# Kernel optimization log

Measured on AMD Instinct MI355X. Metric: run time of the kernel, lower is better.

The kernel has to match this reference:

```python
import jax, jax.numpy as jnp
import numpy as np

N_BLADES = 32  # Cl(4,1) has 2^5 = 32 basis blades


def _gp_sign_bitwise(a, b):
    """Sign of e_a * e_b in Cl(4,1) via bitwise swap counting (numpy, static)."""
    a = np.asarray(a, dtype=np.int64)
    b = np.asarray(b, dtype=np.int64)
    a, b = np.broadcast_arrays(a, b)
    swaps = np.zeros(a.shape, dtype=np.int64)
    for i in range(5):
        b_has_i = (b >> i) & 1
        mask_gt = (~((1 << (i + 1)) - 1)) & 31
        val = a & mask_gt
        pc = (val & 1) + ((val >> 1) & 1) + ((val >> 2) & 1) + ((val >> 3) & 1) + ((val >> 4) & 1)
        swaps += b_has_i * pc
    comm_sign = np.where(swaps % 2 == 0, 1.0, -1.0)
    metric_sign = np.where(((a & 16) & (b & 16)) > 0, -1.0, 1.0)
    return (comm_sign * metric_sign).astype(np.float32)


_M = np.arange(N_BLADES)
PERM = (_M[:, None] ^ _M[None, :]).astype(np.int32)        # PERM[k, m] = m ^ k
SIGNS = _gp_sign_bitwise(_M[None, :], PERM)                 # sign(m, m^k), [32, 32]
PERM_J = jnp.asarray(PERM)
SIGNS_J = jnp.asarray(SIGNS)


def setup_inputs() -> dict:
    key = jax.random.key(0)
    kx, kw = jax.random.split(key)
    B, In, Out = 1024, 256, 256
    x = jax.random.normal(kx, (B, In, N_BLADES), dtype=jnp.float32)
    std = 0.5 / (In * N_BLADES) ** 0.5
    weight = jax.random.normal(kw, (Out, In, N_BLADES), dtype=jnp.float32) * std
    return {"x": x, "weight": weight}


def reference(x, weight):
    # x: [B, In, 32], weight: [Out, In, 32]
    # out[b, o, k] = sum_{i, m} x[b, i, m^k] * sign(m, m^k) * w[o, i, m]
    x_g = x[..., PERM_J] * SIGNS_J                 # [B, In, 32(k), 32(m)]
    out = jnp.einsum('bikm,oim->bok', x_g, weight)  # [B, Out, 32]
    return out
```

## Files before the change

### kernel.cpp

```cpp
#include <hip/hip_runtime.h>

typedef __attribute__((ext_vector_type(8))) short bf16x8;
typedef __attribute__((ext_vector_type(16))) float f32x16;
typedef __attribute__((ext_vector_type(8))) unsigned short ushort8;

#define N_BLADES 32
#define B_DIM 1024
#define IN_DIM 256
#define OUT_DIM 256
#define K_DIM (IN_DIM * N_BLADES)
#define N_DIM (OUT_DIM * N_BLADES)


__device__ __forceinline__ unsigned short f2bf(float f) {
    unsigned int u = __float_as_uint(f);
    u = (u + 0x7fff + ((u >> 16) & 1)) >> 16;
    return (unsigned short)u;
}

__device__ __forceinline__ float gp_sign(int a, int b) {
    int swaps = 0;
#pragma unroll
    for (int i = 0; i < 5; ++i) {
        int mask = (~((1 << (i + 1)) - 1)) & 31;
        swaps += ((b >> i) & 1) * __popc(a & mask);
    }
    float s = (swaps & 1) ? -1.0f : 1.0f;
    if (a & b & 16) s = -s;
    return s;
}

__device__ __forceinline__ void gload_lds16(const void* g, void* l) {
    __builtin_amdgcn_global_load_lds(
        (const __attribute__((address_space(1))) unsigned int*)g,
        (__attribute__((address_space(3))) unsigned int*)l, 16, 0, 0);
}

#define FENCE() asm volatile("" ::: "memory")
#define BAR()    { FENCE(); __builtin_amdgcn_s_barrier(); FENCE(); }
#define SCHED0() __builtin_amdgcn_sched_barrier(0)
#define LGKM(n)  { asm volatile("s_waitcnt lgkmcnt(" #n ")" ::: "memory"); }
#define VMC(n)   { asm volatile("s_waitcnt vmcnt(" #n ")" ::: "memory"); }

__global__ __launch_bounds__(256) void cast_kernel(const float4* __restrict__ x,
                                                   unsigned short* __restrict__ xb) {
    int t = blockIdx.x * 256 + threadIdx.x;
    float4 a = x[t * 2];
    float4 b = x[t * 2 + 1];
    ushort8 pk;
    pk[0] = f2bf(a.x); pk[1] = f2bf(a.y); pk[2] = f2bf(a.z); pk[3] = f2bf(a.w);
    pk[4] = f2bf(b.x); pk[5] = f2bf(b.y); pk[6] = f2bf(b.z); pk[7] = f2bf(b.w);
    *(ushort8*)(xb + (size_t)t * 8) = pk;
}

__device__ __forceinline__ bf16x8 shuffle_sign(bf16x8 v, int jx,
                                               unsigned int m0, unsigned int m1,
                                               unsigned int m2, unsigned int m3) {
    union { bf16x8 v8; unsigned int w[4]; } a, b;
    a.v8 = v;
    int s = jx >> 1;
    unsigned int t0 = (s & 1) ? a.w[1] : a.w[0];
    unsigned int t1 = (s & 1) ? a.w[0] : a.w[1];
    unsigned int t2 = (s & 1) ? a.w[3] : a.w[2];
    unsigned int t3 = (s & 1) ? a.w[2] : a.w[3];
    unsigned int u0 = (s & 2) ? t2 : t0;
    unsigned int u1 = (s & 2) ? t3 : t1;
    unsigned int u2 = (s & 2) ? t0 : t2;
    unsigned int u3 = (s & 2) ? t1 : t3;
    if (jx & 1) {
        u0 = (u0 >> 16) | (u0 << 16);
        u1 = (u1 >> 16) | (u1 << 16);
        u2 = (u2 >> 16) | (u2 << 16);
        u3 = (u3 >> 16) | (u3 << 16);
    }
    b.w[0] = u0 ^ m0; b.w[1] = u1 ^ m1; b.w[2] = u2 ^ m2; b.w[3] = u3 ^ m3;
    return b.v8;
}


#define ROWB 16384

__global__ __launch_bounds__(512, 1) void gemm_ko32_kernel(const unsigned short* __restrict__ xb,
                                                           const unsigned short* __restrict__ wb,
                                                           float* __restrict__ Cws) {
    __shared__ char lds[163840];

    const int tid  = threadIdx.x;
    const int lane = tid & 63;
    const int wid  = tid >> 6;
    const int wr   = wid >> 2;
    const int wc   = wid & 3;
    const int l31  = lane & 31;
    const int l5   = lane >> 5;
    const int swzf = (l31 & 7) << 4;

    const int  kblk = blockIdx.x;
    const long row0 = (long)blockIdx.y * 128;
    const int  jx   = kblk & 7;
    const int  khi  = kblk & 24;

    const int rowA = tid >> 2;
    const int h0   = (2 * tid) & 7;
    const int q0 = h0 & 3, q1 = (h0 + 1) & 3;
    const int aoff0 = ((h0 >> 2) * 64) + (((q0 * 8) ^ khi) * 2);
    const int aoff1 = (((h0 + 1) >> 2) * 64) + (((q1 * 8) ^ khi) * 2);
    const int aswz  = (rowA & 7) << 4;
    const int adst0 = rowA * 128 + ((h0 * 16) ^ aswz);
    const int adst1 = rowA * 128 + (((h0 + 1) * 16) ^ aswz);
    const char* aSrcK = (const char*)xb + (row0 + rowA) * ROWB;

    unsigned int mA00, mA01, mA02, mA03, mA10, mA11, mA12, mA13;
    {
        unsigned int mk[2][4];
#pragma unroll
        for (int u = 0; u < 2; ++u) {
            int q = u ? q1 : q0;
#pragma unroll
            for (int w_ = 0; w_ < 4; ++w_) {
                unsigned int mw = 0;
#pragma unroll
                for (int e2 = 0; e2 < 2; ++e2) {
                    int m = 8 * q + 2 * w_ + e2;
                    if (gp_sign(m, m ^ kblk) < 0.0f) mw |= 0x8000u << (16 * e2);
                }
                mk[u][w_] = mw;
            }
        }
        mA00 = mk[0][0]; mA01 = mk[0][1]; mA02 = mk[0][2]; mA03 = mk[0][3];
        mA10 = mk[1][0]; mA11 = mk[1][1]; mA12 = mk[1][2]; mA13 = mk[1][3];
    }

    const int  tid16 = tid * 16;
    const char* bSrc = (const char*)wb + (long)(tid >> 3) * ROWB
                       + (((tid & 7) * 16) ^ (((tid >> 3) & 7) << 4));

    const int aRdB = (wr * 64 + l31) * 128;
    const int bRdB = (wc * 64 + l31) * 128;
    const int col0_ = ((0 * 32) + l5 * 16) ^ swzf;
    const int col1_ = ((1 * 32) + l5 * 16) ^ swzf;
    const int col2_ = ((2 * 32) + l5 * 16) ^ swzf;
    const int col3_ = ((3 * 32) + l5 * 16) ^ swzf;

#define B_STAGE(br, kpb) { \
    _Pragma("unroll") for (int n = 0; n < 4; ++n) \
        gload_lds16(bSrc + (long)n * (64L * ROWB) + (kpb), \
                    lds + 32768 + (br) * 32768 + n * 8192 + tid16); }
#define A_LOAD_E(kpb) { \
    rAe0 = *(const bf16x8*)(aSrcK + (kpb) + aoff0); \
    rAe1 = *(const bf16x8*)(aSrcK + (kpb) + aoff1); }
#define A_LOAD_O(kpb) { \
    rAo0 = *(const bf16x8*)(aSrcK + (kpb) + aoff0); \
    rAo1 = *(const bf16x8*)(aSrcK + (kpb) + aoff1); }
#define A_WRITE_E(ab) { \
    bf16x8 s0_ = shuffle_sign(rAe0, jx, mA00, mA01, mA02, mA03); \
    bf16x8 s1_ = shuffle_sign(rAe1, jx, mA10, mA11, mA12, mA13); \
    *(bf16x8*)(lds + (ab) * 16384 + adst0) = s0_; \
    *(bf16x8*)(lds + (ab) * 16384 + adst1) = s1_; }
#define A_WRITE_O(ab) { \
    bf16x8 s0_ = shuffle_sign(rAo0, jx, mA00, mA01, mA02, mA03); \
    bf16x8 s1_ = shuffle_sign(rAo1, jx, mA10, mA11, mA12, mA13); \
    *(bf16x8*)(lds + (ab) * 16384 + adst0) = s0_; \
    *(bf16x8*)(lds + (ab) * 16384 + adst1) = s1_; }

#define READ_G0(ab, br) { \
    aG0[0][0] = *(const bf16x8*)(lds + (ab)*16384 + aRdB + 0*4096 + col0_); \
    aG0[0][1] = *(const bf16x8*)(lds + (ab)*16384 + aRdB + 0*4096 + col1_); \
    aG0[1][0] = *(const bf16x8*)(lds + (ab)*16384 + aRdB + 1*4096 + col0_); \
    aG0[1][1] = *(const bf16x8*)(lds + (ab)*16384 + aRdB + 1*4096 + col1_); \
    bG0[0][0] = *(const bf16x8*)(lds + 32768 + (br)*32768 + bRdB + 0*4096 + col0_); \
    bG0[0][1] = *(const bf16x8*)(lds + 32768 + (br)*32768 + bRdB + 0*4096 + col1_); \
    bG0[1][0] = *(const bf16x8*)(lds + 32768 + (br)*32768 + bRdB + 1*4096 + col0_); \
    bG0[1][1] = *(const bf16x8*)(lds + 32768 + (br)*32768 + bRdB + 1*4096 + col1_); }
#define READ_G1(ab, br) { \
    aG1[0][0] = *(const bf16x8*)(lds + (ab)*16384 + aRdB + 0*4096 + col2_); \
    aG1[0][1] = *(const bf16x8*)(lds + (ab)*16384 + aRdB + 0*4096 + col3_); \
    aG1[1][0] = *(const bf16x8*)(lds + (ab)*16384 + aRdB + 1*4096 + col2_); \
    aG1[1][1] = *(const bf16x8*)(lds + (ab)*16384 + aRdB + 1*4096 + col3_); \
    bG1[0][0] = *(const bf16x8*)(lds + 32768 + (br)*32768 + bRdB + 0*4096 + col2_); \
    bG1[0][1] = *(const bf16x8*)(lds + 32768 + (br)*32768 + bRdB + 0*4096 + col3_); \
    bG1[1][0] = *(const bf16x8*)(lds + 32768 + (br)*32768 + bRdB + 1*4096 + col2_); \
    bG1[1][1] = *(const bf16x8*)(lds + 32768 + (br)*32768 + bRdB + 1*4096 + col3_); }
#define MFG0() \
    _Pragma("unroll") for (int s = 0; s < 2; ++s) \
    _Pragma("unroll") for (int mt = 0; mt < 2; ++mt) \
    _Pragma("unroll") for (int nt = 0; nt < 2; ++nt) \
        acc[mt][nt] = __builtin_amdgcn_mfma_f32_32x32x16_bf16(aG0[mt][s], bG0[nt][s], acc[mt][nt], 0, 0, 0);
#define MFG1() \
    _Pragma("unroll") for (int s = 0; s < 2; ++s) \
    _Pragma("unroll") for (int mt = 0; mt < 2; ++mt) \
    _Pragma("unroll") for (int nt = 0; nt < 2; ++nt) \
        acc[mt][nt] = __builtin_amdgcn_mfma_f32_32x32x16_bf16(aG1[mt][s], bG1[nt][s], acc[mt][nt], 0, 0, 0);

    f32x16 acc[2][2];
#pragma unroll
    for (int mt = 0; mt < 2; ++mt)
#pragma unroll
        for (int nt = 0; nt < 2; ++nt) acc[mt][nt] = (f32x16)0.0f;

    bf16x8 rAe0, rAe1, rAo0, rAo1;
    bf16x8 aG0[2][2], bG0[2][2], aG1[2][2], bG1[2][2];

    A_LOAD_E(0);
    SCHED0();
    B_STAGE(0, 0);
    B_STAGE(1, 128);
    SCHED0();
    VMC(8);
    A_WRITE_E(0);
    SCHED0();
    A_LOAD_O(128);
    SCHED0();
    B_STAGE(2, 256);
    SCHED0();
    VMC(6);
    LGKM(0);
    BAR();

#define TILE32(AB, ABN, BR, BRS, ALOAD, AWRITE, Texp) { \
    const int T_ = (Texp); \
    const int kAr = ((T_ + 2) & 127) << 7; \
    const int kBg = ((T_ + 3) & 127) << 7; \
    READ_G0(AB, BR); \
    SCHED0(); \
    READ_G1(AB, BR); \
    SCHED0(); \
    ALOAD(kAr);             \
    SCHED0(); \
    B_STAGE(BRS, kBg);      \
    SCHED0(); \
    LGKM(8); MFG0(); \
    VMC(10);                \
    AWRITE(ABN); \
    SCHED0(); \
    LGKM(2); MFG1(); \
    LGKM(0); \
    VMC(6);                 \
    BAR(); }

    for (int t = 0; t < 32; ++t) {
        const int T4 = t * 4;
        TILE32(0, 1, 0, 3, A_LOAD_E, A_WRITE_O, T4);
        TILE32(1, 0, 1, 0, A_LOAD_O, A_WRITE_E, T4 + 1);
        TILE32(0, 1, 2, 1, A_LOAD_E, A_WRITE_O, T4 + 2);
        TILE32(1, 0, 3, 2, A_LOAD_O, A_WRITE_E, T4 + 3);
    }

#pragma unroll
    for (int mt = 0; mt < 2; ++mt)
#pragma unroll
        for (int nt = 0; nt < 2; ++nt) {
            long c = (long)kblk * 256 + wc * 64 + nt * 32 + l31;
#pragma unroll
            for (int r = 0; r < 16; ++r) {
                int  rl = (r & 3) + 8 * (r >> 2) + 4 * l5;
                long rb = row0 + wr * 64 + mt * 32 + rl;
                Cws[rb * N_DIM + c] = acc[mt][nt][r];
            }
        }

#undef B_STAGE
#undef A_LOAD_E
#undef A_LOAD_O
#undef A_WRITE_E
#undef A_WRITE_O
#undef READ_G0
#undef READ_G1
#undef MFG0
#undef MFG1
#undef TILE32
}

__global__ __launch_bounds__(256) void transpose_kernel(const float* __restrict__ Cws,
                                                        float* __restrict__ out) {
    __shared__ float t[32 * 260];
    const int tid = threadIdx.x;
    const long b  = blockIdx.x;
    const float4* src = (const float4*)(Cws + b * N_DIM);
    float4*       dst = (float4*)(out + b * N_DIM);
#pragma unroll
    for (int r = 0; r < 8; ++r) {
        int f = tid + r * 256;
        float4 v = src[f];
        int k  = f >> 6;
        int c4 = (f & 63) * 4;
        *(float4*)&t[k * 260 + c4] = v;
    }
    __syncthreads();
#pragma unroll
    for (int r = 0; r < 8; ++r) {
        int g  = tid + r * 256;
        int o  = g >> 3;
        int k0 = (g & 7) * 4;
        float4 v;
        v.x = t[(k0 + 0) * 260 + o];
        v.y = t[(k0 + 1) * 260 + o];
        v.z = t[(k0 + 2) * 260 + o];
        v.w = t[(k0 + 3) * 260 + o];
        dst[g] = v;
    }
}

__global__ __launch_bounds__(256) void fallback_gp_kernel(const float* __restrict__ x,
                                                          const float* __restrict__ w,
                                                          float* __restrict__ out) {
    __shared__ float xs[IN_DIM * 32];
    __shared__ float tab[1024];
    int tid = threadIdx.x;
    for (int idx = tid; idx < 1024; idx += 256) {
        int m = idx >> 5, k = idx & 31;
        tab[idx] = gp_sign(m, m ^ k);
    }
    int b = blockIdx.x;
    const float4* xrow = (const float4*)(x + (long)b * K_DIM);
    float4* xs4 = (float4*)xs;
    for (int idx = tid; idx < 2048; idx += 256) xs4[idx] = xrow[idx];
    __syncthreads();

    int wid = tid >> 6, lane = tid & 63;
    int o = blockIdx.y * 8 + wid;
    int k = lane & 31, half = lane >> 5;
    float acc = 0.f;
    const float* wrow = w + (long)o * K_DIM + half * 4096;
    for (int i = 0; i < 128; ++i) {
        int ib = (half * 128 + i) * 32;
#pragma unroll
        for (int m = 0; m < 32; ++m) {
            acc += xs[ib + (m ^ k)] * tab[m * 32 + k] * wrow[i * 32 + m];
        }
    }
    acc += __shfl_down(acc, 32);
    if (half == 0) out[((long)b * OUT_DIM + o) * 32 + k] = acc;
}

extern "C" void kernel_launch(void* const* d_in, const int* in_sizes, int n_in,
                              void* d_out, int out_size, void* d_ws, size_t ws_size,
                              hipStream_t stream) {
    const float* x = (const float*)d_in[0];
    const float* w = (const float*)d_in[1];
    float* out = (float*)d_out;

    const size_t xb_bytes  = (size_t)B_DIM * K_DIM * 2;
    const size_t wb_bytes  = (size_t)OUT_DIM * IN_DIM * 32 * 2;
    const size_t cw_bytes  = (size_t)B_DIM * N_DIM * 4;
    const size_t need = xb_bytes + wb_bytes + cw_bytes;

    if (ws_size >= need) {
        unsigned short* xbp = (unsigned short*)d_ws;
        unsigned short* wbp = (unsigned short*)((char*)d_ws + xb_bytes);
        float*          cws = (float*)((char*)d_ws + xb_bytes + wb_bytes);

        cast_kernel<<<dim3(4096), dim3(256), 0, stream>>>((const float4*)x, xbp);
        cast_kernel<<<dim3(1024), dim3(256), 0, stream>>>((const float4*)w, wbp);
        gemm_ko32_kernel<<<dim3(32, 8), dim3(512), 0, stream>>>(xbp, wbp, cws);
        transpose_kernel<<<dim3(B_DIM), dim3(256), 0, stream>>>(cws, out);
    } else {
        fallback_gp_kernel<<<dim3(B_DIM, OUT_DIM / 8), dim3(256), 0, stream>>>(x, w, out);
    }
}
```

Before: 176.9 us.

## Switch LDS tiles to MFMA-fragment-major layout, dropping XOR swizzle

Reorganizes the shared-memory layout of the A and B tiles so each MFMA operand fragment is stored contiguously (lane-major, 16 bytes per lane). This drops the XOR-swizzled addressing. It also changes how global loads map threads to rows and columns, so each thread handles one row chunk with a single set of sign masks. The aim is conflict-free, simpler LDS reads with less address arithmetic. The risk is that global loads become less coalesced, since consecutive threads now read different rows, and that LDS write patterns change.

```diff
diff --git a/kernel.cpp b/kernel.cpp
--- a/kernel.cpp
+++ b/kernel.cpp
@@ -92,94 +92,80 @@
     const int wc   = wid & 3;
     const int l31  = lane & 31;
     const int l5   = lane >> 5;
-    const int swzf = (l31 & 7) << 4;
 
     const int  kblk = blockIdx.x;
     const long row0 = (long)blockIdx.y * 128;
     const int  jx   = kblk & 7;
-    const int  khi  = kblk & 24;
-
-    const int rowA = tid >> 2;
-    const int h0   = (2 * tid) & 7;
-    const int q0 = h0 & 3, q1 = (h0 + 1) & 3;
-    const int aoff0 = ((h0 >> 2) * 64) + (((q0 * 8) ^ khi) * 2);
-    const int aoff1 = (((h0 + 1) >> 2) * 64) + (((q1 * 8) ^ khi) * 2);
-    const int aswz  = (rowA & 7) << 4;
-    const int adst0 = rowA * 128 + ((h0 * 16) ^ aswz);
-    const int adst1 = rowA * 128 + (((h0 + 1) * 16) ^ aswz);
-    const char* aSrcK = (const char*)xb + (row0 + rowA) * ROWB;
-
-    unsigned int mA00, mA01, mA02, mA03, mA10, mA11, mA12, mA13;
+    const int  kq   = (kblk >> 3) & 3;
+
+    const int rA = tid & 127;
+    const int c0 = tid >> 7;
+    const char* aSrcK = (const char*)xb + (row0 + rA) * ROWB;
+    const int aoffB = ((c0 ^ kq) * 16);
+    const int adst0 = (rA >> 5) * 4096 + c0 * 512 + (rA & 31) * 16;
+
+    unsigned int mk0, mk1, mk2, mk3;
     {
-        unsigned int mk[2][4];
-#pragma unroll
-        for (int u = 0; u < 2; ++u) {
-            int q = u ? q1 : q0;
-#pragma unroll
-            for (int w_ = 0; w_ < 4; ++w_) {
-                unsigned int mw = 0;
-#pragma unroll
-                for (int e2 = 0; e2 < 2; ++e2) {
-                    int m = 8 * q + 2 * w_ + e2;
-                    if (gp_sign(m, m ^ kblk) < 0.0f) mw |= 0x8000u << (16 * e2);
-                }
-                mk[u][w_] = mw;
+        unsigned int mw[4];
+#pragma unroll
+        for (int w_ = 0; w_ < 4; ++w_) {
+            unsigned int m_ = 0;
+#pragma unroll
+            for (int e2 = 0; e2 < 2; ++e2) {
+                int m = 8 * c0 + 2 * w_ + e2;
+                if (gp_sign(m, m ^ kblk) < 0.0f) m_ |= 0x8000u << (16 * e2);
             }
+            mw[w_] = m_;
         }
-        mA00 = mk[0][0]; mA01 = mk[0][1]; mA02 = mk[0][2]; mA03 = mk[0][3];
-        mA10 = mk[1][0]; mA11 = mk[1][1]; mA12 = mk[1][2]; mA13 = mk[1][3];
+        mk0 = mw[0]; mk1 = mw[1]; mk2 = mw[2]; mk3 = mw[3];
     }
 
     const int  tid16 = tid * 16;
-    const char* bSrc = (const char*)wb + (long)(tid >> 3) * ROWB
-                       + (((tid & 7) * 16) ^ (((tid >> 3) & 7) << 4));
-
-    const int aRdB = (wr * 64 + l31) * 128;
-    const int bRdB = (wc * 64 + l31) * 128;
-    const int col0_ = ((0 * 32) + l5 * 16) ^ swzf;
-    const int col1_ = ((1 * 32) + l5 * 16) ^ swzf;
-    const int col2_ = ((2 * 32) + l5 * 16) ^ swzf;
-    const int col3_ = ((3 * 32) + l5 * 16) ^ swzf;
+    const char* bSrc = (const char*)wb + (long)((tid >> 8) * 32 + (tid & 31)) * ROWB
+                       + ((tid >> 5) & 7) * 16;
+
+    const int aL = (wr * 2) * 4096 + l5 * 512 + l31 * 16;
+    const int bL = 32768 + (wc * 2) * 4096 + l5 * 512 + l31 * 16;
 
 #define B_STAGE(br, kpb) { \
     _Pragma("unroll") for (int n = 0; n < 4; ++n) \
         gload_lds16(bSrc + (long)n * (64L * ROWB) + (kpb), \
                     lds + 32768 + (br) * 32768 + n * 8192 + tid16); }
 #define A_LOAD_E(kpb) { \
-    rAe0 = *(const bf16x8*)(aSrcK + (kpb) + aoff0); \
-    rAe1 = *(const bf16x8*)(aSrcK + (kpb) + aoff1); }
+    rAe0 = *(const bf16x8*)(aSrcK + (kpb) + aoffB); \
+    rAe1 = *(const bf16x8*)(aSrcK + (kpb) + aoffB + 64); }
 #define A_LOAD_O(kpb) { \
-    rAo0 = *(const bf16x8*)(aSrcK + (kpb) + aoff0); \
-    rAo1 = *(const bf16x8*)(aSrcK + (kpb) + aoff1); }
+    rAo0 = *(const bf16x8*)(aSrcK + (kpb) + aoffB); \
+    rAo1 = *(const bf16x8*)(aSrcK + (kpb) + aoffB + 64); }
 #define A_WRITE_E(ab) { \
-    bf16x8 s0_ = shuffle_sign(rAe0, jx, mA00, mA01, mA02, mA03); \
-    bf16x8 s1_ = shuffle_sign(rAe1, jx, mA10, mA11, mA12, mA13); \
+    bf16x8 s0_ = shuffle_sign(rAe0, jx, mk0, mk1, mk2, mk3); \
+    bf16x8 s1_ = shuffle_sign(rAe1, jx, mk0, mk1, mk2, mk3); \
     *(bf16x8*)(lds + (ab) * 16384 + adst0) = s0_; \
-    *(bf16x8*)(lds + (ab) * 16384 + adst1) = s1_; }
+    *(bf16x8*)(lds + (ab) * 16384 + adst0 + 2048) = s1_; }
 #define A_WRITE_O(ab) { \
-    bf16x8 s0_ = shuffle_sign(rAo0, jx, mA00, mA01, mA02, mA03); \
-    bf16x8 s1_ = shuffle_sign(rAo1, jx, mA10, mA11, mA12, mA13); \
+    bf16x8 s0_ = shuffle_sign(rAo0, jx, mk0, mk1, mk2, mk3); \
+    bf16x8 s1_ = shuffle_sign(rAo1, jx, mk0, mk1, mk2, mk3); \
     *(bf16x8*)(lds + (ab) * 16384 + adst0) = s0_; \
-    *(bf16x8*)(lds + (ab) * 16384 + adst1) = s1_; }
+    *(bf16x8*)(lds + (ab) * 16384 + adst0 + 2048) = s1_; }
 
 #define READ_G0(ab, br) { \
-    aG0[0][0] = *(const bf16x8*)(lds + (ab)*16384 + aRdB + 0*4096 + col0_); \
-    aG0[0][1] = *(const bf16x8*)(lds + (ab)*16384 + aRdB + 0*4096 + col1_); \
-    aG0[1][0] = *(const bf16x8*)(lds + (ab)*16384 + aRdB + 1*4096 + col0_); \
-    aG0[1][1] = *(const bf16x8*)(lds + (ab)*16384 + aRdB + 1*4096 + col1_); \
-    bG0[0][0] = *(const bf16x8*)(lds + 32768 + (br)*32768 + bRdB + 0*4096 + col0_); \
-    bG0[0][1] = *(const bf16x8*)(lds + 32768 + (br)*32768 + bRdB + 0*4096 + col1_); \
-    bG0[1][0] = *(const bf16x8*)(lds + 32768 + (br)*32768 + bRdB + 1*4096 + col0_); \
-    bG0[1][1] = *(const bf16x8*)(lds + 32768 + (br)*32768 + bRdB + 1*4096 + col1_); }
+    aG0[0][0] = *(const bf16x8*)(lds + (ab)*16384 + aL + 0*4096 + 0*1024); \
+    aG0[0][1] = *(const bf16x8*)(lds + (ab)*16384 + aL + 0*4096 + 1*1024); \
+    aG0[1][0] = *(const bf16x8*)(lds + (ab)*16384 + aL + 1*4096 + 0*1024); \
+    aG0[1][1] = *(const bf16x8*)(lds + (ab)*16384 + aL + 1*4096 + 1*1024); \
+    bG0[0][0] = *(const bf16x8*)(lds + (br)*32768 + bL + 0*4096 + 0*1024); \
+    bG0[0][1] = *(const bf16x8*)(lds + (br)*32768 + bL + 0*4096 + 1*1024); \
+    bG0[1][0] = *(const bf16x8*)(lds + (br)*32768 + bL + 1*4096 + 0*1024); \
+    bG0[1][1] = *(const bf16x8*)(lds + (br)*32768 + bL + 1*4096 + 1*1024); }
 #define READ_G1(ab, br) { \
-    aG1[0][0] = *(const bf16x8*)(lds + (ab)*16384 + aRdB + 0*4096 + col2_); \
-    aG1[0][1] = *(const bf16x8*)(lds + (ab)*16384 + aRdB + 0*4096 + col3_); \
-    aG1[1][0] = *(const bf16x8*)(lds + (ab)*16384 + aRdB + 1*4096 + col2_); \
-    aG1[1][1] = *(const bf16x8*)(lds + (ab)*16384 + aRdB + 1*4096 + col3_); \
-    bG1[0][0] = *(const bf16x8*)(lds + 32768 + (br)*32768 + bRdB + 0*4096 + col2_); \
-    bG1[0][1] = *(const bf16x8*)(lds + 32768 + (br)*32768 + bRdB + 0*4096 + col3_); \
-    bG1[1][0] = *(const bf16x8*)(lds + 32768 + (br)*32768 + bRdB + 1*4096 + col2_); \
-    bG1[1][1] = *(const bf16x8*)(lds + 32768 + (br)*32768 + bRdB + 1*4096 + col3_); }
+    aG1[0][0] = *(const bf16x8*)(lds + (ab)*16384 + aL + 0*4096 + 2*1024); \
+    aG1[0][1] = *(const bf16x8*)(lds + (ab)*16384 + aL + 0*4096 + 3*1024); \
+    aG1[1][0] = *(const bf16x8*)(lds + (ab)*16384 + aL + 1*4096 + 2*1024); \
+    aG1[1][1] = *(const bf16x8*)(lds + (ab)*16384 + aL + 1*4096 + 3*1024); \
+    bG1[0][0] = *(const bf16x8*)(lds + (br)*32768 + bL + 0*4096 + 2*1024); \
+    bG1[0][1] = *(const bf16x8*)(lds + (br)*32768 + bL + 0*4096 + 3*1024); \
+    bG1[1][0] = *(const bf16x8*)(lds + (br)*32768 + bL + 1*4096 + 2*1024); \
+    bG1[1][1] = *(const bf16x8*)(lds + (br)*32768 + bL + 1*4096 + 3*1024); }
 #define MFG0() \
     _Pragma("unroll") for (int s = 0; s < 2; ++s) \
     _Pragma("unroll") for (int mt = 0; mt < 2; ++mt) \
```

New measurement: 244.4 us. +38.1%, slower.
